# Optimization experiments

Hardware: AMD Instinct MI355X
Metric: run time of the kernel (lower is better)

The kernel has to match this reference:

```python
import jax, jax.numpy as jnp
import numpy as np

# Dims: B=batch, C=n_car, N=n_node, E=embed_dim, H=n_heads
B, C, N, E = 64, 8, 512, 512
H = 8
CLIP = 10.0


def setup_inputs() -> dict:
    key = jax.random.key(0)
    ks = jax.random.split(key, 12)
    s = 1.0 / np.sqrt(E)
    mask = jax.random.bernoulli(ks[10], 0.3, (B, C, 1, N))
    mask = mask.at[..., 0].set(False)  # ensure at least one unmasked node per (b,c)
    return {
        "node_embeddings": jax.random.normal(ks[0], (B, N, E), jnp.float32),
        "graph_embedding": jax.random.normal(ks[1], (B, E), jnp.float32),
        "step_context": jax.random.normal(ks[2], (B, C, 1, E + 2), jnp.float32),
        "mask": mask,
        "Wk1": jax.random.normal(ks[3], (E, E), jnp.float32) * s,
        "Wv": jax.random.normal(ks[4], (E, E), jnp.float32) * s,
        "Wk2": jax.random.normal(ks[5], (E, E), jnp.float32) * s,
        "Wq_fixed": jax.random.normal(ks[6], (E, E), jnp.float32) * s,
        "Wout": jax.random.normal(ks[7], (E, E), jnp.float32) * s,
        "Wq_step": jax.random.normal(ks[8], (E, E + 2), jnp.float32) * s,
        "v": jax.random.uniform(ks[9], (E,), jnp.float32, -s, s),
    }


def reference(node_embeddings, graph_embedding, step_context, mask,
              Wk1, Wv, Wk2, Wq_fixed, Wout, Wq_step, v):
    dh = E // H
    neg = jnp.asarray(-1e9, node_embeddings.dtype)

    # compute_static: projections (torch Linear: x @ W.T). K/V/Q_fixed are
    # broadcast over the car dim instead of materialized via .repeat (same math).
    Q_fixed = (graph_embedding @ Wq_fixed.T)[:, None, None, :]  # [B,1,1,E]
    K1 = node_embeddings @ Wk1.T                                 # [B,N,E]
    V = node_embeddings @ Wv.T                                   # [B,N,E]
    K2 = node_embeddings @ Wk2.T                                 # [B,N,E]

    # compute_dynamic
    Q_step = step_context @ Wq_step.T                            # [B,C,1,E]
    Q1 = Q_fixed + Q_step                                        # [B,C,1,E]

    # MHA (need_W=False): split heads, masked scaled dot-product, merge heads.
    qh = Q1.reshape(B, C, H, dh)                                 # q-len 1 squeezed
    kh = K1.reshape(B, N, H, dh)
    vh = V.reshape(B, N, H, dh)
    scores = jnp.einsum('bchd,bnhd->bchn', qh, kh) * (1.0 / np.sqrt(dh))
    m = mask[:, :, 0, :][:, :, None, :]                          # [B,C,1,N]
    scores = jnp.where(m, neg, scores)
    attn = jax.nn.softmax(scores, axis=-1)
    heads = jnp.einsum('bchn,bnhd->bchd', attn, vh).reshape(B, C, E)
    Q3 = heads @ Wout.T                                          # [B,C,E] (Q2.squeeze(2))

    # Pointer logits (SHA): u = tanh(Q_fixed+Q_step) @ v, repeated over E,
    # dotted with K2 => u_scalar * sum_e K2, then tanh-clipped and masked.
    u_scalar = jnp.einsum('bcqe,e->bcq', jnp.tanh(Q1), v)        # [B,C,1]
    k2sum = K2.sum(-1)                                           # [B,N]
    raw = u_scalar * k2sum[:, None, :]                           # [B,C,N]
    logits = CLIP * jnp.tanh(raw * (1.0 / np.sqrt(E)))
    logits = jnp.where(mask[:, :, 0, :], neg, logits)
    logits = logits.reshape(B, C * N)                            # view(batch, -1)
    return logits, Q3
```

## Files before the change

kernel.cpp:

```cpp
#include <hip/hip_runtime.h>


typedef _Float16 f16x8 __attribute__((ext_vector_type(8)));
typedef float f32x4 __attribute__((ext_vector_type(4)));

__device__ __forceinline__ void async16(const void* g, void* l) {
  __builtin_amdgcn_global_load_lds(
      (const __attribute__((address_space(1))) unsigned int*)g,
      (__attribute__((address_space(3))) unsigned int*)l, 16, 0, 0);
}

__device__ __forceinline__ float fast_tanh(float x) {
  float ax = fabsf(x);
  float t = __expf(-2.f * ax);
  float r = (1.f - t) / (1.f + t);
  return copysignf(r, x);
}

__global__ __launch_bounds__(256) void prep_q1(
    const float* __restrict__ Wk1, const float* __restrict__ Wv,
    const float* __restrict__ Wk2, _Float16* __restrict__ W1h,
    _Float16* __restrict__ W2h, float* __restrict__ colsum,
    const float* __restrict__ ge, const float* __restrict__ sc,
    const float* __restrict__ Wqf, const float* __restrict__ Wqs,
    float* __restrict__ Q1) {
  const int bid = blockIdx.x;
  if (bid < 272) {
    if (bid < 16) {
      const int tx = threadIdx.x & 31, ty = threadIdx.x >> 5;
      const int col = bid * 32 + tx;
      float s = 0.f;
#pragma unroll 4
      for (int e = ty * 64; e < ty * 64 + 64; ++e) s += Wk2[e * 512 + col];
      __shared__ float red[8][32];
      red[ty][tx] = s;
      __syncthreads();
      if (ty == 0) {
        float t = 0.f;
#pragma unroll
        for (int g = 0; g < 8; ++g) t += red[g][tx];
        colsum[col] = t;
      }
    } else {
      const int cb = bid - 16;
      const float* src = (cb < 128) ? Wk1 : Wv;
      _Float16* dst = (cb < 128) ? W1h : W2h;
      const size_t off = (size_t)(cb & 127) * 2048 + threadIdx.x * 8;
      float4 a = *(const float4*)(src + off);
      float4 b = *(const float4*)(src + off + 4);
      union { _Float16 h[8]; uint4 u; } pk;
      pk.h[0] = (_Float16)a.x; pk.h[1] = (_Float16)a.y;
      pk.h[2] = (_Float16)a.z; pk.h[3] = (_Float16)a.w;
      pk.h[4] = (_Float16)b.x; pk.h[5] = (_Float16)b.y;
      pk.h[6] = (_Float16)b.z; pk.h[7] = (_Float16)b.w;
      *(uint4*)(dst + off) = pk.u;
    }
    return;
  }

  const int b2 = bid - 272;
  const int mb = b2 & 7, nb = (b2 >> 3) & 7, ks = b2 >> 6;
  const int tid = threadIdx.x;
  const int lane = tid & 63, wave = tid >> 6;
  const int wm = (wave >> 1) * 32, wn = (wave & 1) * 32;

  __shared__ __align__(16) _Float16 As[64][40];
  __shared__ __align__(16) _Float16 Ws[64][40];

  f32x4 acc[2][2] = {};
  const int qd = (lane >> 4) * 8, rr = lane & 15;

  for (int kt = 0; kt < 9; ++kt) {
    const int kb = ks * 288 + kt * 32;
#pragma unroll
    for (int f0 = 0; f0 < 2; ++f0) {
      int f = tid + f0 * 256;
      int r = f >> 3, c4 = (f & 7) * 4;
      int m = mb * 64 + r;
      int e = nb * 64 + r;
#pragma unroll
      for (int j = 0; j < 4; ++j) {
        int k = kb + c4 + j;
        float a = 0.f, w = 0.f;
        if (k < 512) {
          a = ge[(m >> 3) * 512 + k];
          w = Wqf[(size_t)e * 512 + k];
        } else if (k < 1026) {
          a = sc[(size_t)m * 514 + (k - 512)];
          w = Wqs[(size_t)e * 514 + (k - 512)];
        }
        As[r][c4 + j] = (_Float16)a;
        Ws[r][c4 + j] = (_Float16)w;
      }
    }
    __syncthreads();
    f16x8 af[2], bfr[2];
#pragma unroll
    for (int mi = 0; mi < 2; ++mi) af[mi] = *(const f16x8*)&As[wm + mi * 16 + rr][qd];
#pragma unroll
    for (int ni = 0; ni < 2; ++ni) bfr[ni] = *(const f16x8*)&Ws[wn + ni * 16 + rr][qd];
#pragma unroll
    for (int mi = 0; mi < 2; ++mi)
#pragma unroll
      for (int ni = 0; ni < 2; ++ni)
        acc[mi][ni] =
            __builtin_amdgcn_mfma_f32_16x16x32_f16(af[mi], bfr[ni], acc[mi][ni], 0, 0, 0);
    __syncthreads();
  }

  const int col = lane & 15, rq = (lane >> 4) * 4;
#pragma unroll
  for (int mi = 0; mi < 2; ++mi)
#pragma unroll
    for (int ni = 0; ni < 2; ++ni)
#pragma unroll
      for (int r = 0; r < 4; ++r) {
        int m = mb * 64 + wm + mi * 16 + rq + r;
        int e = nb * 64 + wn + ni * 16 + col;
        atomicAdd(&Q1[(size_t)m * 512 + e], acc[mi][ni][r]);
      }
}

__global__ __launch_bounds__(256, 2) void gemm_kv(
    const float* __restrict__ A, const _Float16* __restrict__ W1,
    const _Float16* __restrict__ W2, const float* __restrict__ colsum,
    _Float16* __restrict__ K1, _Float16* __restrict__ Vt,
    float* __restrict__ k2sum) {
  const int flat = (int)(blockIdx.y * 4 + blockIdx.x);
  const int work = (flat & 7) * 128 + (flat >> 3);
  const int nb = work & 3;
  const int mb = work >> 2;
  const int tid = threadIdx.x, lane = tid & 63, wave = tid >> 6;
  const int wm = (wave >> 1) * 64, wn = (wave & 1) * 64;
  const int row0 = mb * 128, col0 = nb * 128;
  const int b = mb >> 2;

  __shared__ __align__(16) _Float16 Ah[128 * 64];
  __shared__ __align__(16) _Float16 Wb[2][2][128 * 64];

  f32x4 acc1[4][4] = {}, acc2[4][4] = {};
  float k2p[4] = {0.f, 0.f, 0.f, 0.f};
  const int q = lane >> 4, rr = lane & 15;
  const int wlr = lane >> 3, wlc = lane & 7;
  const int cswz = wlc ^ wlr;

  const int ar0 = tid >> 3, ac = tid & 7;
  const float* aptr = A + (size_t)(row0 + ar0) * 512 + ac * 8;
  const int aslot = ac ^ (ar0 & 7);

  float4 areg[4][2];
  float4 cs0, cs1;

  auto issue_a = [&](int kt) {
#pragma unroll
    for (int j = 0; j < 4; ++j) {
      const float* gp = aptr + (size_t)j * 32 * 512 + kt * 64;
      areg[j][0] = *(const float4*)gp;
      areg[j][1] = *(const float4*)(gp + 4);
    }
    if (nb == 0) {
      const float* csp = colsum + kt * 64 + ac * 8;
      cs0 = *(const float4*)csp;
      cs1 = *(const float4*)(csp + 4);
    }
  };
  auto issue_w = [&](int kt, int buf) {
    const int kbase = kt * 64;
#pragma unroll
    for (int j = 0; j < 4; ++j) {
      int r = wave * 32 + j * 8 + wlr;
      int ldsrow = (wave * 32 + j * 8) * 64;
      size_t goff = (size_t)(col0 + r) * 512 + kbase + cswz * 8;
      async16(W1 + goff, &Wb[buf][0][ldsrow]);
      async16(W2 + goff, &Wb[buf][1][ldsrow]);
    }
  };
  auto write_a = [&](int kt) {
#pragma unroll
    for (int j = 0; j < 4; ++j) {
      union { _Float16 h[8]; uint4 u; } pk;
      float4 lo = areg[j][0], hi = areg[j][1];
      pk.h[0] = (_Float16)lo.x; pk.h[1] = (_Float16)lo.y;
      pk.h[2] = (_Float16)lo.z; pk.h[3] = (_Float16)lo.w;
      pk.h[4] = (_Float16)hi.x; pk.h[5] = (_Float16)hi.y;
      pk.h[6] = (_Float16)hi.z; pk.h[7] = (_Float16)hi.w;
      *(uint4*)&Ah[(ar0 + 32 * j) * 64 + aslot * 8] = pk.u;
    }
    if (nb == 0) {
#pragma unroll
      for (int j = 0; j < 4; ++j) {
        float4 lo = areg[j][0], hi = areg[j][1];
        k2p[j] += lo.x * cs0.x + lo.y * cs0.y + lo.z * cs0.z + lo.w * cs0.w +
                  hi.x * cs1.x + hi.y * cs1.y + hi.z * cs1.z + hi.w * cs1.w;
      }
    }
  };

  issue_a(0);
  issue_w(0, 0);
  write_a(0);
  __syncthreads();

  for (int kt = 0; kt < 8; ++kt) {
    const int p = kt & 1;
    if (kt < 7) {
      issue_a(kt + 1);
      issue_w(kt + 1, p ^ 1);
    }
#pragma unroll
    for (int k0 = 0; k0 < 64; k0 += 32) {
      const int cb = (k0 >> 3) + q;
      f16x8 af[4], b1[4], b2[4];
#pragma unroll
      for (int mi = 0; mi < 4; ++mi) {
        int ra = wm + mi * 16 + rr;
        af[mi] = *(const f16x8*)&Ah[ra * 64 + (cb ^ (ra & 7)) * 8];
      }
#pragma unroll
      for (int ni = 0; ni < 4; ++ni) {
        int rw = wn + ni * 16 + rr;
        int slot = cb ^ (rw & 7);
        b1[ni] = *(const f16x8*)&Wb[p][0][rw * 64 + slot * 8];
        b2[ni] = *(const f16x8*)&Wb[p][1][rw * 64 + slot * 8];
      }
      __builtin_amdgcn_s_setprio(1);
#pragma unroll
      for (int mi = 0; mi < 4; ++mi)
#pragma unroll
        for (int ni = 0; ni < 4; ++ni) {
          acc1[mi][ni] =
              __builtin_amdgcn_mfma_f32_16x16x32_f16(af[mi], b1[ni], acc1[mi][ni], 0, 0, 0);
          acc2[mi][ni] =
              __builtin_amdgcn_mfma_f32_16x16x32_f16(af[mi], b2[ni], acc2[mi][ni], 0, 0, 0);
        }
      __builtin_amdgcn_s_setprio(0);
    }
    if (kt < 7) {
      __syncthreads();
      write_a(kt + 1);
      __syncthreads();
    }
  }

  if (nb == 0) {
#pragma unroll
    for (int j = 0; j < 4; ++j) {
      float s = k2p[j];
      s += __shfl_xor(s, 1, 8);
      s += __shfl_xor(s, 2, 8);
      s += __shfl_xor(s, 4, 8);
      if (ac == 0) k2sum[row0 + ar0 + 32 * j] = s;
    }
  }

  const int col = lane & 15, rq = (lane >> 4) * 4;
#pragma unroll
  for (int mi = 0; mi < 4; ++mi)
#pragma unroll
    for (int ni = 0; ni < 4; ++ni)
#pragma unroll
      for (int r = 0; r < 4; ++r) {
        size_t m = row0 + wm + mi * 16 + rq + r;
        size_t e = col0 + wn + ni * 16 + col;
        K1[m * 512 + e] = (_Float16)acc1[mi][ni][r];
      }

  _Float16* Vts = &Wb[0][0][0];
#pragma unroll
  for (int mi = 0; mi < 4; ++mi)
#pragma unroll
    for (int ni = 0; ni < 4; ++ni) {
      int n0 = wm + mi * 16 + rq;
      int el = wn + ni * 16 + col;
      int cn = n0 >> 3, half = (n0 >> 2) & 1;
      int slot = cn ^ (el & 7);
      union { _Float16 h[4]; unsigned long long u; } pk;
#pragma unroll
      for (int r = 0; r < 4; ++r) pk.h[r] = (_Float16)acc2[mi][ni][r];
      *(unsigned long long*)&Vts[el * 128 + slot * 8 + half * 4] = pk.u;
    }
  __syncthreads();
  const int nbase = row0 & 511;
#pragma unroll
  for (int i = 0; i < 8; ++i) {
    int f = tid + i * 256;
    int el = f >> 4, c16 = f & 15;
    int slot = c16 ^ (el & 7);
    uint4 val = *(const uint4*)&Vts[el * 128 + slot * 8];
    *(uint4*)(Vt + (size_t)b * 262144 + (size_t)(col0 + el) * 512 + nbase + c16 * 8) = val;
  }
}

__global__ __launch_bounds__(256) void attn_kernel(
    const float* __restrict__ Q1, const _Float16* __restrict__ K1,
    const _Float16* __restrict__ Vt, const int* __restrict__ mask,
    float* __restrict__ heads) {
  const int bid = blockIdx.x;
  const int b = bid >> 3, h = bid & 7;
  const int tid = threadIdx.x, wave = tid >> 6, lane = tid & 63;
  const int q = lane >> 4, cl = lane & 15;

  __shared__ __align__(16) _Float16 buf[2][256 * 64];
  __shared__ __align__(16) _Float16 P[16][264];
  __shared__ float red[4][8];

  f16x8 af[2];
  {
    const float* qp = Q1 + (size_t)(b * 8 + (cl & 7)) * 512 + h * 64 + q * 8;
#pragma unroll
    for (int s = 0; s < 2; ++s) {
      float4 l0 = *(const float4*)(qp + s * 32);
      float4 l1 = *(const float4*)(qp + s * 32 + 4);
      af[s][0] = (_Float16)l0.x; af[s][1] = (_Float16)l0.y;
      af[s][2] = (_Float16)l0.z; af[s][3] = (_Float16)l0.w;
      af[s][4] = (_Float16)l1.x; af[s][5] = (_Float16)l1.y;
      af[s][6] = (_Float16)l1.z; af[s][7] = (_Float16)l1.w;
    }
  }

  const _Float16* Kb = K1 + (size_t)b * 262144 + h * 64;
  const _Float16* Vb = Vt + (size_t)b * 262144 + (size_t)h * 64 * 512;

  auto stage_K = [&](_Float16* dst, int rbase) {
#pragma unroll
    for (int j = 0; j < 8; ++j) {
      int r = wave * 64 + j * 8 + (lane >> 3);
      int cg = (lane & 7) ^ (r & 7);
      async16(Kb + (size_t)(rbase + r) * 512 + cg * 8, &dst[(wave * 64 + j * 8) * 64]);
    }
  };
  auto stage_V = [&](_Float16* dst, int noff) {
#pragma unroll
    for (int j = 0; j < 8; ++j) {
      int r = wave * 16 + j * 2 + (lane >> 5);
      int cg = (lane & 31) ^ (r & 7);
      async16(Vb + (size_t)r * 512 + noff + cg * 8, &dst[(wave * 16 + j * 2) * 256]);
    }
  };

  f32x4 acc[8] = {};
  auto qk_half = [&](const _Float16* src, int h2) {
    __builtin_amdgcn_s_setprio(1);
#pragma unroll
    for (int tt = 0; tt < 4; ++tt) {
      int rn = wave * 64 + tt * 16 + cl;
#pragma unroll
      for (int s = 0; s < 2; ++s) {
        int slot = (s * 4 + q) ^ (cl & 7);
        f16x8 bf = *(const f16x8*)&src[rn * 64 + slot * 8];
        acc[h2 * 4 + tt] =
            __builtin_amdgcn_mfma_f32_16x16x32_f16(af[s], bf, acc[h2 * 4 + tt], 0, 0, 0);
      }
    }
    __builtin_amdgcn_s_setprio(0);
  };

  stage_K(buf[0], 0);
  __syncthreads();
  stage_K(buf[1], 256);
  qk_half(buf[0], 0);
  __syncthreads();
  stage_V(buf[0], 0);
  qk_half(buf[1], 1);
  __syncthreads();
  stage_V(buf[1], 256);

  float gmax[4], rsum[4] = {0.f, 0.f, 0.f, 0.f};
  if (q < 2) {
    float mx[4] = {-3e38f, -3e38f, -3e38f, -3e38f};
#pragma unroll
    for (int t = 0; t < 8; ++t) {
      int n = (t >> 2) * 256 + wave * 64 + (t & 3) * 16 + cl;
#pragma unroll
      for (int r = 0; r < 4; ++r) {
        int c = q * 4 + r;
        float x = mask[(size_t)(b * 8 + c) * 512 + n] ? -1e9f : acc[t][r] * 0.125f;
        acc[t][r] = x;
        mx[r] = fmaxf(mx[r], x);
      }
    }
#pragma unroll
    for (int off = 1; off < 16; off <<= 1)
#pragma unroll
      for (int r = 0; r < 4; ++r) mx[r] = fmaxf(mx[r], __shfl_xor(mx[r], off, 64));
    if (cl == 0)
#pragma unroll
      for (int r = 0; r < 4; ++r) red[wave][q * 4 + r] = mx[r];
  }
  __syncthreads();
  if (q < 2) {
#pragma unroll
    for (int r = 0; r < 4; ++r) {
      int c = q * 4 + r;
      gmax[r] = fmaxf(fmaxf(red[0][c], red[1][c]), fmaxf(red[2][c], red[3][c]));
    }
#pragma unroll
    for (int t = 0; t < 4; ++t) {
      int np = wave * 64 + (t & 3) * 16 + cl;
#pragma unroll
      for (int r = 0; r < 4; ++r) {
        float e = __expf(acc[t][r] - gmax[r]);
        rsum[r] += e;
        P[q * 4 + r][np] = (_Float16)e;
      }
    }
  }
  __syncthreads();

  f32x4 pacc = {};
  const int rn = wave * 16 + cl;
  __builtin_amdgcn_s_setprio(1);
#pragma unroll
  for (int sl = 0; sl < 8; ++sl) {
    int slot = (sl * 4 + q) ^ (cl & 7);
    f16x8 bf = *(const f16x8*)&buf[0][rn * 256 + slot * 8];
    f16x8 pa = *(const f16x8*)&P[cl][sl * 32 + q * 8];
    pacc = __builtin_amdgcn_mfma_f32_16x16x32_f16(pa, bf, pacc, 0, 0, 0);
  }
  __builtin_amdgcn_s_setprio(0);
  __syncthreads();

  if (q < 2) {
#pragma unroll
    for (int t = 4; t < 8; ++t) {
      int np = wave * 64 + (t & 3) * 16 + cl;
#pragma unroll
      for (int r = 0; r < 4; ++r) {
        float e = __expf(acc[t][r] - gmax[r]);
        rsum[r] += e;
        P[q * 4 + r][np] = (_Float16)e;
      }
    }
#pragma unroll
    for (int off = 1; off < 16; off <<= 1)
#pragma unroll
      for (int r = 0; r < 4; ++r) rsum[r] += __shfl_xor(rsum[r], off, 64);
    if (cl == 0)
#pragma unroll
      for (int r = 0; r < 4; ++r) red[wave][q * 4 + r] = rsum[r];
  }
  __syncthreads();

  __builtin_amdgcn_s_setprio(1);
#pragma unroll
  for (int sl = 0; sl < 8; ++sl) {
    int slot = (sl * 4 + q) ^ (cl & 7);
    f16x8 bf = *(const f16x8*)&buf[1][rn * 256 + slot * 8];
    f16x8 pa = *(const f16x8*)&P[cl][sl * 32 + q * 8];
    pacc = __builtin_amdgcn_mfma_f32_16x16x32_f16(pa, bf, pacc, 0, 0, 0);
  }
  __builtin_amdgcn_s_setprio(0);

  if (q < 2) {
#pragma unroll
    for (int r = 0; r < 4; ++r) {
      int c = q * 4 + r;
      float inv = 1.f / (red[0][c] + red[1][c] + red[2][c] + red[3][c]);
      heads[(size_t)(b * 8 + c) * 512 + h * 64 + wave * 16 + cl] = pacc[r] * inv;
    }
  }
}

__global__ __launch_bounds__(256) void out_logits(
    const float* __restrict__ A, const float* __restrict__ W,
    float* __restrict__ C, const float* __restrict__ Q1,
    const float* __restrict__ v, const float* __restrict__ k2s,
    const int* __restrict__ mask, float* __restrict__ out) {
  const int bid = blockIdx.x;
  if (bid < 64) {
    const int mb = bid & 7, nb = bid >> 3;
    const int tid = threadIdx.x;
    const int lane = tid & 63, wave = tid >> 6;
    const int wm = (wave >> 1) * 32, wn = (wave & 1) * 32;

    __shared__ __align__(16) _Float16 As[64][40];
    __shared__ __align__(16) _Float16 Ws[64][40];

    f32x4 acc[2][2] = {};
    const int qd = (lane >> 4) * 8, rr = lane & 15;

    for (int kt = 0; kt < 16; ++kt) {
      const int kb = kt * 32;
#pragma unroll
      for (int f0 = 0; f0 < 2; ++f0) {
        int f = tid + f0 * 256;
        int r = f >> 3, c4 = (f & 7) * 4;
        float4 a = *(const float4*)(A + (size_t)(mb * 64 + r) * 512 + kb + c4);
        float4 w = *(const float4*)(W + (size_t)(nb * 64 + r) * 512 + kb + c4);
        As[r][c4 + 0] = (_Float16)a.x; As[r][c4 + 1] = (_Float16)a.y;
        As[r][c4 + 2] = (_Float16)a.z; As[r][c4 + 3] = (_Float16)a.w;
        Ws[r][c4 + 0] = (_Float16)w.x; Ws[r][c4 + 1] = (_Float16)w.y;
        Ws[r][c4 + 2] = (_Float16)w.z; Ws[r][c4 + 3] = (_Float16)w.w;
      }
      __syncthreads();
      f16x8 af[2], bfr[2];
#pragma unroll
      for (int mi = 0; mi < 2; ++mi) af[mi] = *(const f16x8*)&As[wm + mi * 16 + rr][qd];
#pragma unroll
      for (int ni = 0; ni < 2; ++ni) bfr[ni] = *(const f16x8*)&Ws[wn + ni * 16 + rr][qd];
#pragma unroll
      for (int mi = 0; mi < 2; ++mi)
#pragma unroll
        for (int ni = 0; ni < 2; ++ni)
          acc[mi][ni] =
              __builtin_amdgcn_mfma_f32_16x16x32_f16(af[mi], bfr[ni], acc[mi][ni], 0, 0, 0);
      __syncthreads();
    }

    const int col = lane & 15, rq = (lane >> 4) * 4;
#pragma unroll
    for (int mi = 0; mi < 2; ++mi)
#pragma unroll
      for (int ni = 0; ni < 2; ++ni)
#pragma unroll
        for (int r = 0; r < 4; ++r) {
          int m = mb * 64 + wm + mi * 16 + rq + r;
          int e = nb * 64 + wn + ni * 16 + col;
          C[(size_t)m * 512 + e] = acc[mi][ni][r];
        }
    return;
  }

  const int bc = bid - 64;
  const int b = bc >> 3;
  const int tid = threadIdx.x;
  const int wave = tid >> 6, lane = tid & 63;

  float p = fast_tanh(Q1[(size_t)bc * 512 + tid]) * v[tid] +
            fast_tanh(Q1[(size_t)bc * 512 + tid + 256]) * v[tid + 256];
#pragma unroll
  for (int off = 32; off; off >>= 1) p += __shfl_down(p, off, 64);
  __shared__ float red[4];
  __shared__ float su;
  if (lane == 0) red[wave] = p;
  __syncthreads();
  if (tid == 0) su = red[0] + red[1] + red[2] + red[3];
  __syncthreads();
  const float u = su;

#pragma unroll
  for (int i = 0; i < 2; ++i) {
    int n = tid + i * 256;
    int idx = bc * 512 + n;
    out[idx] = mask[idx] ? -1e9f
                         : 10.f * fast_tanh(u * k2s[b * 512 + n] * 0.04419417382415922f);
  }
}

extern "C" void kernel_launch(void* const* d_in, const int* in_sizes, int n_in,
                              void* d_out, int out_size, void* d_ws, size_t ws_size,
                              hipStream_t stream) {
  const float* ne = (const float*)d_in[0];
  const float* ge = (const float*)d_in[1];
  const float* sc = (const float*)d_in[2];
  const int* mask = (const int*)d_in[3];
  const float* Wk1 = (const float*)d_in[4];
  const float* Wv = (const float*)d_in[5];
  const float* Wk2 = (const float*)d_in[6];
  const float* Wqf = (const float*)d_in[7];
  const float* Wout = (const float*)d_in[8];
  const float* Wqs = (const float*)d_in[9];
  const float* v = (const float*)d_in[10];

  float* logits = (float*)d_out;
  float* q3 = (float*)d_out + 262144;

  char* ws = (char*)d_ws;
  _Float16* K1 = (_Float16*)(ws + 0);
  _Float16* Vt = (_Float16*)(ws + 33554432);
  float* Q1 = (float*)(ws + 67108864);
  float* heads = (float*)(ws + 68157440);
  float* k2sum = (float*)(ws + 69206016);
  float* colsum = (float*)(ws + 69337088);
  _Float16* W1h = (_Float16*)(ws + 69339136);
  _Float16* W2h = (_Float16*)(ws + 69863424);

  hipMemsetAsync(Q1, 0, 1048576, stream);
  prep_q1<<<528, 256, 0, stream>>>(Wk1, Wv, Wk2, W1h, W2h, colsum,
                                   ge, sc, Wqf, Wqs, Q1);
  gemm_kv<<<dim3(4, 256), 256, 0, stream>>>(ne, W1h, W2h, colsum, K1, Vt, k2sum);
  attn_kernel<<<512, 256, 0, stream>>>(Q1, K1, Vt, mask, heads);
  out_logits<<<576, 256, 0, stream>>>(heads, Wout, q3, Q1, v, k2sum, mask, logits);
}
```

Baseline: 209.1 us.

## Pre-convert node embeddings to fp16 and add fp16-input KV GEMM variant

Adds 512 extra blocks to the prep kernel that convert node_embeddings from fp32 to fp16 in workspace. A new gemm_kvh kernel then reads fp16 A tiles (half the global bytes, no in-loop conversion) with double-buffered async weight loads, and folds the k2sum colsum dot into the A write. The fp16 path is used only when the workspace is large enough; otherwise the old kernel runs. The conversion pass adds a full extra read and write of the embeddings before the GEMM.

After: 214.3 us. 2.5% more time.

```diff
diff --git a/kernel.cpp b/kernel.cpp
--- a/kernel.cpp
+++ b/kernel.cpp
@@ -23,7 +23,8 @@
     _Float16* __restrict__ W2h, float* __restrict__ colsum,
     const float* __restrict__ ge, const float* __restrict__ sc,
     const float* __restrict__ Wqf, const float* __restrict__ Wqs,
-    float* __restrict__ Q1) {
+    float* __restrict__ Q1, const float* __restrict__ ne,
+    _Float16* __restrict__ neh) {
   const int bid = blockIdx.x;
   if (bid < 272) {
     if (bid < 16) {
@@ -57,6 +58,23 @@
     }
     return;
   }
+  if (bid >= 528) {
+    const int cb2 = bid - 528;
+    const size_t base = (size_t)cb2 * 32768 + threadIdx.x * 8;
+#pragma unroll
+    for (int j = 0; j < 16; ++j) {
+      size_t idx = base + (size_t)j * 2048;
+      float4 a = *(const float4*)(ne + idx);
+      float4 b = *(const float4*)(ne + idx + 4);
+      union { _Float16 h[8]; uint4 u; } pk;
+      pk.h[0] = (_Float16)a.x; pk.h[1] = (_Float16)a.y;
+      pk.h[2] = (_Float16)a.z; pk.h[3] = (_Float16)a.w;
+      pk.h[4] = (_Float16)b.x; pk.h[5] = (_Float16)b.y;
+      pk.h[6] = (_Float16)b.z; pk.h[7] = (_Float16)b.w;
+      *(uint4*)(neh + idx) = pk.u;
+    }
+    return;
+  }
 
   const int b2 = bid - 272;
   const int mb = b2 & 7, nb = (b2 >> 3) & 7, ks = b2 >> 6;
@@ -250,6 +268,171 @@
       s += __shfl_xor(s, 2, 8);
       s += __shfl_xor(s, 4, 8);
       if (ac == 0) k2sum[row0 + ar0 + 32 * j] = s;
+    }
+  }
+
+  const int col = lane & 15, rq = (lane >> 4) * 4;
+#pragma unroll
+  for (int mi = 0; mi < 4; ++mi)
+#pragma unroll
+    for (int ni = 0; ni < 4; ++ni)
+#pragma unroll
+      for (int r = 0; r < 4; ++r) {
+        size_t m = row0 + wm + mi * 16 + rq + r;
+        size_t e = col0 + wn + ni * 16 + col;
+        K1[m * 512 + e] = (_Float16)acc1[mi][ni][r];
+      }
+
+  _Float16* Vts = &Wb[0][0][0];
+#pragma unroll
+  for (int mi = 0; mi < 4; ++mi)
+#pragma unroll
+    for (int ni = 0; ni < 4; ++ni) {
+      int n0 = wm + mi * 16 + rq;
+      int el = wn + ni * 16 + col;
+      int cn = n0 >> 3, half = (n0 >> 2) & 1;
+      int slot = cn ^ (el & 7);
+      union { _Float16 h[4]; unsigned long long u; } pk;
+#pragma unroll
+      for (int r = 0; r < 4; ++r) pk.h[r] = (_Float16)acc2[mi][ni][r];
+      *(unsigned long long*)&Vts[el * 128 + slot * 8 + half * 4] = pk.u;
+    }
+  __syncthreads();
+  const int nbase = row0 & 511;
+#pragma unroll
+  for (int i = 0; i < 8; ++i) {
+    int f = tid + i * 256;
+    int el = f >> 4, c16 = f & 15;
+    int slot = c16 ^ (el & 7);
+    uint4 val = *(const uint4*)&Vts[el * 128 + slot * 8];
+    *(uint4*)(Vt + (size_t)b * 262144 + (size_t)(col0 + el) * 512 + nbase + c16 * 8) = val;
+  }
+}
+
+__global__ __launch_bounds__(256, 2) void gemm_kvh(
+    const _Float16* __restrict__ A, const _Float16* __restrict__ W1,
+    const _Float16* __restrict__ W2, const float* __restrict__ colsum,
+    _Float16* __restrict__ K1, _Float16* __restrict__ Vt,
+    float* __restrict__ k2sum) {
+  const int flat = (int)(blockIdx.y * 4 + blockIdx.x);
+  const int work = (flat & 7) * 128 + (flat >> 3);
+  const int nb = work & 3;
+  const int mb = work >> 2;
+  const int tid = threadIdx.x, lane = tid & 63, wave = tid >> 6;
+  const int wm = (wave >> 1) * 64, wn = (wave & 1) * 64;
+  const int row0 = mb * 128, col0 = nb * 128;
+  const int b = mb >> 2;
+
+  __shared__ __align__(16) _Float16 Ah[128 * 64];
+  __shared__ __align__(16) _Float16 Wb[2][2][128 * 64];
+
+  f32x4 acc1[4][4] = {}, acc2[4][4] = {};
+  float k2p[4] = {0.f, 0.f, 0.f, 0.f};
+  const int q = lane >> 4, rr = lane & 15;
+  const int wlr = lane >> 3, wlc = lane & 7;
+  const int cswz = wlc ^ wlr;
+
+  const int ac = tid & 7;
+  uint4 areg[4];
+  float4 cs0, cs1;
+
+  auto issue_a = [&](int kt) {
+#pragma unroll
+    for (int j = 0; j < 4; ++j) {
+      int c = tid + j * 256;
+      int row = c >> 3;
+      areg[j] = *(const uint4*)(A + (size_t)(row0 + row) * 512 + kt * 64 + ac * 8);
+    }
+    if (nb == 0) {
+      const float* csp = colsum + kt * 64 + ac * 8;
+      cs0 = *(const float4*)csp;
+      cs1 = *(const float4*)(csp + 4);
+    }
+  };
+  auto issue_w = [&](int kt, int buf) {
+    const int kbase = kt * 64;
+#pragma unroll
+    for (int j = 0; j < 4; ++j) {
+      int r = wave * 32 + j * 8 + wlr;
+      int ldsrow = (wave * 32 + j * 8) * 64;
+      size_t goff = (size_t)(col0 + r) * 512 + kbase + cswz * 8;
+      async16(W1 + goff, &Wb[buf][0][ldsrow]);
+      async16(W2 + goff, &Wb[buf][1][ldsrow]);
+    }
+  };
+  auto write_a = [&]() {
+#pragma unroll
+    for (int j = 0; j < 4; ++j) {
+      int c = tid + j * 256;
+      int row = c >> 3;
+      *(uint4*)&Ah[row * 64 + (ac ^ (row & 7)) * 8] = areg[j];
+    }
+    if (nb == 0) {
+#pragma unroll
+      for (int j = 0; j < 4; ++j) {
+        const _Float16* hv = (const _Float16*)&areg[j];
+        k2p[j] += (float)hv[0] * cs0.x + (float)hv[1] * cs0.y +
+                  (float)hv[2] * cs0.z + (float)hv[3] * cs0.w +
+                  (float)hv[4] * cs1.x + (float)hv[5] * cs1.y +
+                  (float)hv[6] * cs1.z + (float)hv[7] * cs1.w;
+      }
+    }
+  };
+
+  issue_a(0);
+  issue_w(0, 0);
+  write_a();
+  __syncthreads();
+
+  for (int kt = 0; kt < 8; ++kt) {
+    const int p = kt & 1;
+    if (kt < 7) {
+      issue_a(kt + 1);
+      issue_w(kt + 1, p ^ 1);
+    }
+#pragma unroll
+    for (int k0 = 0; k0 < 64; k0 += 32) {
+      const int cb = (k0 >> 3) + q;
+      f16x8 af[4], b1[4], b2[4];
+#pragma unroll
+      for (int mi = 0; mi < 4; ++mi) {
+        int ra = wm + mi * 16 + rr;
+        af[mi] = *(const f16x8*)&Ah[ra * 64 + (cb ^ (ra & 7)) * 8];
+      }
+#pragma unroll
+      for (int ni = 0; ni < 4; ++ni) {
+        int rw = wn + ni * 16 + rr;
+        int slot = cb ^ (rw & 7);
+        b1[ni] = *(const f16x8*)&Wb[p][0][rw * 64 + slot * 8];
+        b2[ni] = *(const f16x8*)&Wb[p][1][rw * 64 + slot * 8];
+      }
+      __builtin_amdgcn_s_setprio(1);
+#pragma unroll
+      for (int mi = 0; mi < 4; ++mi)
+#pragma unroll
+        for (int ni = 0; ni < 4; ++ni) {
+          acc1[mi][ni] =
+              __builtin_amdgcn_mfma_f32_16x16x32_f16(af[mi], b1[ni], acc1[mi][ni], 0, 0, 0);
+          acc2[mi][ni] =
+              __builtin_amdgcn_mfma_f32_16x16x32_f16(af[mi], b2[ni], acc2[mi][ni], 0, 0, 0);
+        }
+      __builtin_amdgcn_s_setprio(0);
+    }
+    if (kt < 7) {
+      __syncthreads();
+      write_a();
+      __syncthreads();
+    }
+  }
+
+  if (nb == 0) {
+#pragma unroll
+    for (int j = 0; j < 4; ++j) {
+      float s = k2p[j];
+      s += __shfl_xor(s, 1, 8);
+      s += __shfl_xor(s, 2, 8);
+      s += __shfl_xor(s, 4, 8);
+      if (ac == 0) k2sum[row0 + ((tid + j * 256) >> 3)] = s;
     }
   }
 
@@ -574,11 +757,18 @@
   float* colsum = (float*)(ws + 69337088);
   _Float16* W1h = (_Float16*)(ws + 69339136);
   _Float16* W2h = (_Float16*)(ws + 69863424);
+  _Float16* neh = (_Float16*)(ws + 70387712);
+
+  const bool f16A = ws_size >= (size_t)70387712 + 33554432;
 
   hipMemsetAsync(Q1, 0, 1048576, stream);
-  prep_q1<<<528, 256, 0, stream>>>(Wk1, Wv, Wk2, W1h, W2h, colsum,
-                                   ge, sc, Wqf, Wqs, Q1);
-  gemm_kv<<<dim3(4, 256), 256, 0, stream>>>(ne, W1h, W2h, colsum, K1, Vt, k2sum);
+  prep_q1<<<f16A ? 1040 : 528, 256, 0, stream>>>(
+      Wk1, Wv, Wk2, W1h, W2h, colsum, ge, sc, Wqf, Wqs, Q1, ne, neh);
+  if (f16A) {
+    gemm_kvh<<<dim3(4, 256), 256, 0, stream>>>(neh, W1h, W2h, colsum, K1, Vt, k2sum);
+  } else {
+    gemm_kv<<<dim3(4, 256), 256, 0, stream>>>(ne, W1h, W2h, colsum, K1, Vt, k2sum);
+  }
   attn_kernel<<<512, 256, 0, stream>>>(Q1, K1, Vt, mask, heads);
   out_logits<<<576, 256, 0, stream>>>(heads, Wout, q3, Q1, v, k2sum, mask, logits);
 }
```
